# Kernel tuning notes

Hardware: AMD Instinct MI355X
Metric: run time of the kernel (lower is better)

The kernel has to match this reference:

```python
import jax, jax.numpy as jnp
import numpy as np

NEG_SLOPE = 0.01  # nn.LeakyReLU default

def leaky(x):
    return jnp.where(x >= 0, x, NEG_SLOPE * x)

def setup_inputs() -> dict:
    key = jax.random.key(0)
    ks = jax.random.split(key, 10)
    N, E, IN_DIM, OUT_DIM = 100000, 1600000, 128, 128
    indices = jax.random.randint(ks[0], (2, E), 0, N, dtype=jnp.int64 if jax.config.jax_enable_x64 else jnp.int32)
    features = jax.random.normal(ks[1], (N, IN_DIM), dtype=jnp.float32)
    s = 1.0 / np.sqrt(IN_DIM)
    W_att_w = jax.random.uniform(ks[2], (OUT_DIM, IN_DIM), minval=-s, maxval=s)
    W_att_b = jax.random.uniform(ks[3], (OUT_DIM,), minval=-s, maxval=s)
    W1_w = jax.random.uniform(ks[4], (OUT_DIM, IN_DIM), minval=-s, maxval=s)
    W1_b = jax.random.uniform(ks[5], (OUT_DIM,), minval=-s, maxval=s)
    W2_w = jax.random.uniform(ks[6], (OUT_DIM, OUT_DIM), minval=-s, maxval=s)
    W2_b = jax.random.uniform(ks[7], (OUT_DIM,), minval=-s, maxval=s)
    # xavier_uniform for a: gain*sqrt(6/(fan_in+fan_out)), fan_in=2*OUT_DIM, fan_out=1
    lim = float(np.sqrt(6.0 / (2 * OUT_DIM + 1)))
    a = jax.random.uniform(ks[8], (2 * OUT_DIM, 1), minval=-lim, maxval=lim)
    return {"indices": indices, "features": features, "num_nodes": N,
            "W_att_w": W_att_w, "W_att_b": W_att_b, "W1_w": W1_w, "W1_b": W1_b,
            "W2_w": W2_w, "W2_b": W2_b, "a": a}

def reference(indices, features, num_nodes, W_att_w, W_att_b, W1_w, W1_b, W2_w, W2_b, a):
    src, dst = indices[0], indices[1]
    out_dim = W_att_w.shape[0]
    # h_trans = W_att(features)
    h_trans = features @ W_att_w.T + W_att_b  # [N, D]
    # cat([src_h, dst_h]) @ a  ==  src_h @ a[:D] + dst_h @ a[D:]  (avoids materializing cat)
    a_src, a_dst = a[:out_dim], a[out_dim:]
    logits = leaky(h_trans[src] @ a_src + h_trans[dst] @ a_dst)  # [E, 1]
    # edge softmax over incoming edges of each dst (raw exp, as in original)
    exp_l = jnp.exp(logits)
    denom = jax.ops.segment_sum(exp_l, dst, num_segments=num_nodes)  # [N, 1]
    alpha = exp_l / (denom[dst] + 1e-9)  # [E, 1]
    # sparse.mm(adj_att, W1(features)) == segment_sum of alpha * msg[src] over dst
    h_msg = features @ W1_w.T + W1_b  # [N, D]
    h_neigh = jax.ops.segment_sum(alpha * h_msg[src], dst, num_segments=num_nodes)  # [N, D]
    h_self = features  # in_dim == out_dim branch
    term1 = h_self + h_neigh
    term2 = (h_self * h_neigh) @ W2_w.T + W2_b
    return leaky(term1 + term2)
```

## Files before the change

### kernel.cpp

```cpp
#include <hip/hip_runtime.h>

#define D 128
typedef __attribute__((ext_vector_type(8))) short short8;
typedef __attribute__((ext_vector_type(4))) float f32x4;

__device__ __forceinline__ float leaky(float x){ return x >= 0.f ? x : 0.01f*x; }
__device__ __forceinline__ unsigned short f2bf(float x){
    unsigned u = __float_as_uint(x);
    u = (u + 0x7fffu + ((u>>16)&1u)) >> 16;
    return (unsigned short)u;
}

__global__ void k_prep(const float* __restrict__ Ww, const float* __restrict__ Wb,
                       const float* __restrict__ a, float* __restrict__ v,
                       const float* __restrict__ W1, const float* __restrict__ W2,
                       unsigned short* __restrict__ W1b, unsigned short* __restrict__ W2b){
    int b = blockIdx.x;
    if(b < 64){
        int i = b*256 + threadIdx.x;
        W1b[i] = f2bf(W1[i]);
        W2b[i] = f2bf(W2[i]);
        return;
    }
    int i = threadIdx.x; if(i >= 128) return;
    float vs=0.f, vd=0.f;
    for (int o=0;o<D;++o){ float w = Ww[o*D+i]; vs = fmaf(w, a[o], vs); vd = fmaf(w, a[D+o], vd); }
    v[i]=vs; v[D+i]=vd;
    if(i==0){
        float cs=0.f,cd=0.f;
        for(int o=0;o<D;++o){ cs=fmaf(Wb[o],a[o],cs); cd=fmaf(Wb[o],a[D+o],cd); }
        v[256]=cs; v[257]=cd;
    }
}

__global__ __launch_bounds__(256) void k_msgscal(const float* __restrict__ F,
        const unsigned short* __restrict__ W1b, const float* __restrict__ b1,
        const float* __restrict__ v, unsigned short* __restrict__ Hp,
        float* __restrict__ ss, float* __restrict__ sd, int N){
    const int lane = threadIdx.x & 63;
    const int wid  = blockIdx.x*4 + (threadIdx.x>>6);
    const int nw   = gridDim.x*4;
    const int t = lane & 15, g = lane >> 4;
    short8 wf[4][8];
    #pragma unroll
    for(int kk=0;kk<4;++kk)
      #pragma unroll
      for(int j=0;j<8;++j)
        wf[kk][j] = *(const short8*)(W1b + (size_t)(j*16+t)*D + kk*32 + g*8);
    float bb[8];
    #pragma unroll
    for(int j=0;j<8;++j) bb[j] = b1[j*16+t];
    const float c_s = v[256], c_d = v[257];
    const int Mt = (N+15)>>4;
    for(int rt = wid; rt < Mt; rt += nw){
        int row0 = rt*16 + t;
        int row = row0 < N ? row0 : N-1;
        const float* fr = F + (size_t)row*D + g*8;
        f32x4 acc[8];
        #pragma unroll
        for(int j=0;j<8;++j) acc[j] = (f32x4){0.f,0.f,0.f,0.f};
        float ds = 0.f, dd = 0.f;
        #pragma unroll
        for(int kk=0;kk<4;++kk){
            f32x4 lo = *(const f32x4*)(fr + kk*32);
            f32x4 hi = *(const f32x4*)(fr + kk*32 + 4);
            f32x4 vsl = *(const f32x4*)(v + kk*32 + g*8);
            f32x4 vsh = *(const f32x4*)(v + kk*32 + g*8 + 4);
            f32x4 vdl = *(const f32x4*)(v + D + kk*32 + g*8);
            f32x4 vdh = *(const f32x4*)(v + D + kk*32 + g*8 + 4);
            #pragma unroll
            for(int q=0;q<4;++q){
                ds = fmaf(lo[q], vsl[q], ds); ds = fmaf(hi[q], vsh[q], ds);
                dd = fmaf(lo[q], vdl[q], dd); dd = fmaf(hi[q], vdh[q], dd);
            }
            short8 af;
            af[0]=(short)f2bf(lo[0]); af[1]=(short)f2bf(lo[1]);
            af[2]=(short)f2bf(lo[2]); af[3]=(short)f2bf(lo[3]);
            af[4]=(short)f2bf(hi[0]); af[5]=(short)f2bf(hi[1]);
            af[6]=(short)f2bf(hi[2]); af[7]=(short)f2bf(hi[3]);
            #pragma unroll
            for(int j=0;j<8;++j)
                acc[j] = __builtin_amdgcn_mfma_f32_16x16x32_bf16(af, wf[kk][j], acc[j], 0,0,0);
        }
        ds += __shfl_xor(ds,16); ds += __shfl_xor(ds,32);
        dd += __shfl_xor(dd,16); dd += __shfl_xor(dd,32);
        if(g==0 && row0 < N){ ss[row0] = ds + c_s; sd[row0] = dd + c_d; }
        #pragma unroll
        for(int r=0;r<4;++r){
            int rr = rt*16 + g*4 + r;
            if(rr < N){
                short8 h;
                #pragma unroll
                for(int j=0;j<8;++j) h[j] = (short)f2bf(acc[j][r] + bb[j]);
                *(short8*)(Hp + (size_t)rr*D + t*8) = h;
            }
        }
    }
}

__global__ __launch_bounds__(256) void k_bcount(const int* __restrict__ dst,
        unsigned* __restrict__ M, int E, int NB, int CHUNK){
    __shared__ unsigned h[1600];
    for(int i=threadIdx.x;i<NB;i+=256) h[i]=0u;
    __syncthreads();
    int s = blockIdx.x*CHUNK;
    int e = s+CHUNK < E ? s+CHUNK : E;
    for(int i=s+(int)threadIdx.x;i<e;i+=256) atomicAdd(&h[((unsigned)dst[i])>>6],1u);
    __syncthreads();
    for(int i=threadIdx.x;i<NB;i+=256) M[(size_t)i*gridDim.x + blockIdx.x] = h[i];
}

__global__ __launch_bounds__(256) void k_scanA(const unsigned* __restrict__ M,
        unsigned* __restrict__ bsum, int n){
    __shared__ unsigned lds[4];
    int base = blockIdx.x*4096 + threadIdx.x*16;
    unsigned s=0;
    #pragma unroll
    for(int k=0;k<16;++k){ int i=base+k; if(i<n) s+=M[i]; }
    #pragma unroll
    for(int o=1;o<64;o<<=1) s += __shfl_xor(s,o);
    if((threadIdx.x&63)==0) lds[threadIdx.x>>6]=s;
    __syncthreads();
    if(threadIdx.x==0) bsum[blockIdx.x] = lds[0]+lds[1]+lds[2]+lds[3];
}

__global__ __launch_bounds__(256) void k_scanB(unsigned* __restrict__ bsum, int nb){
    __shared__ unsigned lds[4];
    int t = threadIdx.x;
    int chunk = (nb+255)/256;
    int s0 = t*chunk, s1 = s0+chunk < nb ? s0+chunk : nb;
    unsigned tsum=0;
    for(int i=s0;i<s1;++i) tsum += bsum[i];
    unsigned x=tsum;
    #pragma unroll
    for(int o=1;o<64;o<<=1){ unsigned y=__shfl_up(x,(unsigned)o); if((t&63)>=o) x+=y; }
    if((t&63)==63) lds[t>>6]=x;
    __syncthreads();
    unsigned woff=0;
    for(int w=0;w<(t>>6);++w) woff+=lds[w];
    unsigned run = woff + (x - tsum);
    for(int i=s0;i<s1;++i){ unsigned vv=bsum[i]; bsum[i]=run; run+=vv; }
}

__global__ __launch_bounds__(256) void k_scanC(const unsigned* __restrict__ M,
        const unsigned* __restrict__ bsum, unsigned* __restrict__ Msc, int n){
    __shared__ unsigned lds[4];
    int t = threadIdx.x;
    int base = blockIdx.x*4096 + t*16;
    unsigned v[16]; unsigned tsum=0;
    #pragma unroll
    for(int k=0;k<16;++k){ int i=base+k; v[k]=(i<n)?M[i]:0u; tsum+=v[k]; }
    unsigned x=tsum;
    #pragma unroll
    for(int o=1;o<64;o<<=1){ unsigned y=__shfl_up(x,(unsigned)o); if((t&63)>=o) x+=y; }
    if((t&63)==63) lds[t>>6]=x;
    __syncthreads();
    unsigned woff = bsum[blockIdx.x];
    for(int w=0;w<(t>>6);++w) woff+=lds[w];
    unsigned run = woff + (x - tsum);
    #pragma unroll
    for(int k=0;k<16;++k){ int i=base+k; if(i<n) Msc[i]=run; run+=v[k]; }
}

__global__ __launch_bounds__(256) void k_bscatter(const int* __restrict__ src,
        const int* __restrict__ dst, const unsigned* __restrict__ Msc,
        uint2* __restrict__ ew, int E, int NB, int CHUNK){
    __shared__ unsigned hoff[1600];
    int blk = blockIdx.x, NBLKg = gridDim.x;
    for(int i=threadIdx.x;i<NB;i+=256) hoff[i] = Msc[(size_t)i*NBLKg + blk];
    __syncthreads();
    int s = blk*CHUNK;
    int e = s+CHUNK < E ? s+CHUNK : E;
    for(int i=s+(int)threadIdx.x;i<e;i+=256){
        int d = dst[i];
        unsigned p = atomicAdd(&hoff[((unsigned)d)>>6], 1u);
        ew[p] = make_uint2((unsigned)src[i], (unsigned)d);
    }
}

__global__ __launch_bounds__(256) void k_fine(const uint2* __restrict__ ew,
        const unsigned* __restrict__ Msc, const float* __restrict__ ss,
        const float* __restrict__ sdv, uint2* __restrict__ ewp,
        unsigned* __restrict__ offs, int N, int NB, int NBLKg, int E){
    __shared__ unsigned cA[64], cB[64], loff[64];
    __shared__ float sdl[64];
    __shared__ unsigned begS, endS;
    int b = blockIdx.x;
    int dbase = b<<6;
    if(threadIdx.x==0){
        begS = Msc[(size_t)b*NBLKg];
        endS = (b+1 < NB) ? Msc[(size_t)(b+1)*NBLKg] : (unsigned)E;
    }
    if(threadIdx.x<64){
        cA[threadIdx.x]=0u; cB[threadIdx.x]=0u;
        int dd = dbase + (int)threadIdx.x;
        sdl[threadIdx.x] = (dd<N) ? sdv[dd] : 0.f;
    }
    __syncthreads();
    const unsigned beg = begS, end = endS;
    for(unsigned i=beg+threadIdx.x; i<end; i+=256)
        atomicAdd(&cA[ew[i].y & 63], 1u);
    __syncthreads();
    if(threadIdx.x<64){
        unsigned c = cA[threadIdx.x];
        unsigned x = c;
        #pragma unroll
        for(int o=1;o<64;o<<=1){ unsigned y = __shfl_up(x,(unsigned)o); if((int)threadIdx.x>=o) x += y; }
        loff[threadIdx.x] = x - c;
        int dd = dbase + (int)threadIdx.x;
        if(dd < N) offs[dd] = beg + x - c;
    }
    if(b==0 && threadIdx.x==64) offs[N] = (unsigned)E;
    if(b==0 && threadIdx.x>=80 && threadIdx.x<96)
        ewp[E + (threadIdx.x-80)] = make_uint2(0u, 0u);
    __syncthreads();
    for(unsigned i=beg+threadIdx.x; i<end; i+=256){
        uint2 p = ew[i];
        unsigned dl = p.y & 63;
        float w = __expf(leaky(ss[p.x] + sdl[dl]));
        unsigned r = atomicAdd(&cB[dl], 1u);
        ewp[beg + loff[dl] + r] = make_uint2(p.x, __float_as_uint(w));
    }
}

__device__ __forceinline__ void fma8(float* acc, uint4 u, float w){
    acc[0]=fmaf(w,__uint_as_float(u.x<<16),acc[0]);
    acc[1]=fmaf(w,__uint_as_float(u.x&0xffff0000u),acc[1]);
    acc[2]=fmaf(w,__uint_as_float(u.y<<16),acc[2]);
    acc[3]=fmaf(w,__uint_as_float(u.y&0xffff0000u),acc[3]);
    acc[4]=fmaf(w,__uint_as_float(u.z<<16),acc[4]);
    acc[5]=fmaf(w,__uint_as_float(u.z&0xffff0000u),acc[5]);
    acc[6]=fmaf(w,__uint_as_float(u.w<<16),acc[6]);
    acc[7]=fmaf(w,__uint_as_float(u.w&0xffff0000u),acc[7]);
}

__global__ __launch_bounds__(256) void k_gather(const unsigned* __restrict__ off,
        const uint2* __restrict__ ewp, const unsigned short* __restrict__ Hp,
        float* __restrict__ out, int N){
    const int wv = threadIdx.x>>6, l = threadIdx.x&63;
    const int d = blockIdx.x*4 + wv;
    if(d>=N) return;
    const int g = l>>4, t = l&15;
    const unsigned kb = off[d], ke = off[d+1];
    const unsigned toff = (unsigned)t*16u;
    float acc[8];
    #pragma unroll
    for(int j=0;j<8;++j) acc[j]=0.f;
    float den = 0.f;

    unsigned e = kb + g;
    uint2 p0 = ewp[e];
    uint4 u0 = *(const uint4*)((const char*)Hp + ((p0.x<<8) + toff));
    uint2 p1 = ewp[e+4];
    uint4 u1 = *(const uint4*)((const char*)Hp + ((p1.x<<8) + toff));
    while(e < ke){
        float w0 = __uint_as_float(p0.y);
        fma8(acc, u0, w0);
        p0 = ewp[e+8];
        u0 = *(const uint4*)((const char*)Hp + ((p0.x<<8) + toff));
        float w1 = (e+4 < ke) ? __uint_as_float(p1.y) : 0.f;
        fma8(acc, u1, w1);
        p1 = ewp[e+12];
        u1 = *(const uint4*)((const char*)Hp + ((p1.x<<8) + toff));
        den += w0 + w1;
        e += 8;
    }
    #pragma unroll
    for(int j=0;j<8;++j){
        acc[j] += __shfl_xor(acc[j],16);
        acc[j] += __shfl_xor(acc[j],32);
    }
    den += __shfl_xor(den,16);
    den += __shfl_xor(den,32);
    float inv = 1.f/(den + 1e-9f);
    int c = g*32 + t;
    out[(size_t)d*D + c]      = acc[g*2]  * inv;
    out[(size_t)d*D + c + 16] = acc[g*2+1]* inv;
}

__global__ __launch_bounds__(256) void k_final(const float* __restrict__ F,
        const unsigned short* __restrict__ W2b, const float* __restrict__ b2,
        float* __restrict__ out, int N){
    const int lane = threadIdx.x & 63;
    const int wid  = blockIdx.x*4 + (threadIdx.x>>6);
    const int nw   = gridDim.x*4;
    const int t = lane & 15, g = lane >> 4;
    short8 wf[4][8];
    #pragma unroll
    for(int kk=0;kk<4;++kk)
      #pragma unroll
      for(int j=0;j<8;++j)
        wf[kk][j] = *(const short8*)(W2b + (size_t)(j*16+t)*D + kk*32 + g*8);
    float bb[8];
    #pragma unroll
    for(int j=0;j<8;++j) bb[j] = b2[j*16+t];
    const int Mt = (N+15)>>4;
    for(int rt = wid; rt < Mt; rt += nw){
        int row = rt*16 + t; if(row>=N) row = N-1;
        const float* fr = F   + (size_t)row*D + g*8;
        const float* hr = out + (size_t)row*D + g*8;
        f32x4 acc[8];
        #pragma unroll
        for(int j=0;j<8;++j) acc[j] = (f32x4){0.f,0.f,0.f,0.f};
        #pragma unroll
        for(int kk=0;kk<4;++kk){
            f32x4 flo = *(const f32x4*)(fr + kk*32);
            f32x4 fhi = *(const f32x4*)(fr + kk*32 + 4);
            f32x4 hlo = *(const f32x4*)(hr + kk*32);
            f32x4 hhi = *(const f32x4*)(hr + kk*32 + 4);
            short8 af;
            af[0]=(short)f2bf(flo[0]*hlo[0]); af[1]=(short)f2bf(flo[1]*hlo[1]);
            af[2]=(short)f2bf(flo[2]*hlo[2]); af[3]=(short)f2bf(flo[3]*hlo[3]);
            af[4]=(short)f2bf(fhi[0]*hhi[0]); af[5]=(short)f2bf(fhi[1]*hhi[1]);
            af[6]=(short)f2bf(fhi[2]*hhi[2]); af[7]=(short)f2bf(fhi[3]*hhi[3]);
            #pragma unroll
            for(int j=0;j<8;++j)
                acc[j] = __builtin_amdgcn_mfma_f32_16x16x32_bf16(af, wf[kk][j], acc[j], 0,0,0);
        }
        #pragma unroll
        for(int r=0;r<4;++r){
            int rr = rt*16 + g*4 + r;
            if(rr < N){
                #pragma unroll
                for(int j=0;j<8;++j){
                    int c = j*16 + t;
                    float f = F[(size_t)rr*D + c];
                    float h = out[(size_t)rr*D + c];
                    float val = f + h + acc[j][r] + bb[j];
                    out[(size_t)rr*D + c] = leaky(val);
                }
            }
        }
    }
}

extern "C" void kernel_launch(void* const* d_in, const int* in_sizes, int n_in,
                              void* d_out, int out_size, void* d_ws, size_t ws_size,
                              hipStream_t stream) {
    const int*   idx  = (const int*)  d_in[0];
    const float* F    = (const float*)d_in[1];
    const float* Waw  = (const float*)d_in[3];
    const float* Wab  = (const float*)d_in[4];
    const float* W1w  = (const float*)d_in[5];
    const float* W1b  = (const float*)d_in[6];
    const float* W2w  = (const float*)d_in[7];
    const float* W2b  = (const float*)d_in[8];
    const float* a    = (const float*)d_in[9];
    float* out = (float*)d_out;

    const int E = in_sizes[0]/2;
    const int N = in_sizes[1]/D;
    const int* srcp = idx;
    const int* dstp = idx + E;

    const int NBLK = 256;
    const int CHUNK = (E + NBLK - 1)/NBLK;
    const int NB = (N + 63)/64;
    const int NT = NB*NBLK;
    const int NSB = (NT + 4095)/4096;

    uint2*    ew   = (uint2*)d_ws;
    uint2*    ewp  = ew + E;
    unsigned short* Hp  = (unsigned short*)(ewp + E + 16);
    unsigned short* W1c = Hp + (size_t)N*D;
    unsigned short* W2c = W1c + 16384;
    float*    ss   = (float*)(W2c + 16384);
    float*    sd   = ss + N;
    float*    v    = sd + N;
    unsigned* M    = (unsigned*)(v + 320);
    unsigned* Msc  = M + NT;
    unsigned* bsum = Msc + NT + 2;
    unsigned* offs = bsum + NSB + 2;

    const int Mt = (N+15)/16;
    const int GG = (Mt+7)/8;

    k_prep    <<<65, 256, 0, stream>>>(Waw, Wab, a, v, W1w, W2w, W1c, W2c);
    k_msgscal <<<GG, 256, 0, stream>>>(F, W1c, W1b, v, Hp, ss, sd, N);
    k_bcount  <<<NBLK, 256, 0, stream>>>(dstp, M, E, NB, CHUNK);
    k_scanA   <<<NSB, 256, 0, stream>>>(M, bsum, NT);
    k_scanB   <<<1, 256, 0, stream>>>(bsum, NSB);
    k_scanC   <<<NSB, 256, 0, stream>>>(M, bsum, Msc, NT);
    k_bscatter<<<NBLK, 256, 0, stream>>>(srcp, dstp, Msc, ew, E, NB, CHUNK);
    k_fine    <<<NB, 256, 0, stream>>>(ew, Msc, ss, sd, ewp, offs, N, NB, NBLK, E);
    k_gather  <<<(N+3)/4, 256, 0, stream>>>(offs, ewp, Hp, out, N);
    k_final   <<<GG, 256, 0, stream>>>(F, W2c, W2b, out, N);
}
```

Before: 220.8 us.

## Fuse gather with final MFMA epilogue, fold scanB into scanC, move exp to scatter

```diff
diff --git a/kernel.cpp b/kernel.cpp
--- a/kernel.cpp
+++ b/kernel.cpp
@@ -124,66 +124,54 @@
     if(threadIdx.x==0) bsum[blockIdx.x] = lds[0]+lds[1]+lds[2]+lds[3];
 }
 
-__global__ __launch_bounds__(256) void k_scanB(unsigned* __restrict__ bsum, int nb){
+__global__ __launch_bounds__(256) void k_scanC(const unsigned* __restrict__ M,
+        const unsigned* __restrict__ bsum, unsigned* __restrict__ Msc, int n, int nsb){
     __shared__ unsigned lds[4];
+    __shared__ unsigned ps[2];
     int t = threadIdx.x;
-    int chunk = (nb+255)/256;
-    int s0 = t*chunk, s1 = s0+chunk < nb ? s0+chunk : nb;
-    unsigned tsum=0;
-    for(int i=s0;i<s1;++i) tsum += bsum[i];
+    unsigned pv = (t < nsb && t < (int)blockIdx.x) ? bsum[t] : 0u;
+    #pragma unroll
+    for(int o=1;o<64;o<<=1) pv += __shfl_xor(pv,o);
+    if((t&63)==0 && t<128) ps[t>>6]=pv;
+    int base = blockIdx.x*4096 + t*16;
+    unsigned v[16]; unsigned tsum=0;
+    #pragma unroll
+    for(int k=0;k<16;++k){ int i=base+k; v[k]=(i<n)?M[i]:0u; tsum+=v[k]; }
     unsigned x=tsum;
     #pragma unroll
     for(int o=1;o<64;o<<=1){ unsigned y=__shfl_up(x,(unsigned)o); if((t&63)>=o) x+=y; }
     if((t&63)==63) lds[t>>6]=x;
     __syncthreads();
-    unsigned woff=0;
-    for(int w=0;w<(t>>6);++w) woff+=lds[w];
-    unsigned run = woff + (x - tsum);
-    for(int i=s0;i<s1;++i){ unsigned vv=bsum[i]; bsum[i]=run; run+=vv; }
-}
-
-__global__ __launch_bounds__(256) void k_scanC(const unsigned* __restrict__ M,
-        const unsigned* __restrict__ bsum, unsigned* __restrict__ Msc, int n){
-    __shared__ unsigned lds[4];
-    int t = threadIdx.x;
-    int base = blockIdx.x*4096 + t*16;
-    unsigned v[16]; unsigned tsum=0;
-    #pragma unroll
-    for(int k=0;k<16;++k){ int i=base+k; v[k]=(i<n)?M[i]:0u; tsum+=v[k]; }
-    unsigned x=tsum;
-    #pragma unroll
-    for(int o=1;o<64;o<<=1){ unsigned y=__shfl_up(x,(unsigned)o); if((t&63)>=o) x+=y; }
-    if((t&63)==63) lds[t>>6]=x;
-    __syncthreads();
-    unsigned woff = bsum[blockIdx.x];
-    for(int w=0;w<(t>>6);++w) woff+=lds[w];
-    unsigned run = woff + (x - tsum);
+    unsigned run = ps[0]+ps[1];
+    for(int w=0;w<(t>>6);++w) run += lds[w];
+    run += (x - tsum);
     #pragma unroll
     for(int k=0;k<16;++k){ int i=base+k; if(i<n) Msc[i]=run; run+=v[k]; }
 }
 
 __global__ __launch_bounds__(256) void k_bscatter(const int* __restrict__ src,
         const int* __restrict__ dst, const unsigned* __restrict__ Msc,
+        const float* __restrict__ ss, const float* __restrict__ sdv,
         uint2* __restrict__ ew, int E, int NB, int CHUNK){
     __shared__ unsigned hoff[1600];
     int blk = blockIdx.x, NBLKg = gridDim.x;
     for(int i=threadIdx.x;i<NB;i+=256) hoff[i] = Msc[(size_t)i*NBLKg + blk];
     __syncthreads();
-    int s = blk*CHUNK;
-    int e = s+CHUNK < E ? s+CHUNK : E;
-    for(int i=s+(int)threadIdx.x;i<e;i+=256){
+    int s0 = blk*CHUNK;
+    int e1 = s0+CHUNK < E ? s0+CHUNK : E;
+    for(int i=s0+(int)threadIdx.x;i<e1;i+=256){
         int d = dst[i];
+        int s = src[i];
+        float w = __expf(leaky(ss[s] + sdv[d]));
         unsigned p = atomicAdd(&hoff[((unsigned)d)>>6], 1u);
-        ew[p] = make_uint2((unsigned)src[i], (unsigned)d);
+        ew[p] = make_uint2(((unsigned)s<<6)|((unsigned)d&63u), __float_as_uint(w));
     }
 }
 
 __global__ __launch_bounds__(256) void k_fine(const uint2* __restrict__ ew,
-        const unsigned* __restrict__ Msc, const float* __restrict__ ss,
-        const float* __restrict__ sdv, uint2* __restrict__ ewp,
+        const unsigned* __restrict__ Msc, uint2* __restrict__ ewp,
         unsigned* __restrict__ offs, int N, int NB, int NBLKg, int E){
     __shared__ unsigned cA[64], cB[64], loff[64];
-    __shared__ float sdl[64];
     __shared__ unsigned begS, endS;
     int b = blockIdx.x;
     int dbase = b<<6;
@@ -191,15 +179,11 @@
         begS = Msc[(size_t)b*NBLKg];
         endS = (b+1 < NB) ? Msc[(size_t)(b+1)*NBLKg] : (unsigned)E;
     }
-    if(threadIdx.x<64){
-        cA[threadIdx.x]=0u; cB[threadIdx.x]=0u;
-        int dd = dbase + (int)threadIdx.x;
-        sdl[threadIdx.x] = (dd<N) ? sdv[dd] : 0.f;
-    }
+    if(threadIdx.x<64){ cA[threadIdx.x]=0u; cB[threadIdx.x]=0u; }
     __syncthreads();
     const unsigned beg = begS, end = endS;
     for(unsigned i=beg+threadIdx.x; i<end; i+=256)
-        atomicAdd(&cA[ew[i].y & 63], 1u);
+        atomicAdd(&cA[ew[i].x & 63u], 1u);
     __syncthreads();
     if(threadIdx.x<64){
         unsigned c = cA[threadIdx.x];
@@ -216,10 +200,9 @@
     __syncthreads();
     for(unsigned i=beg+threadIdx.x; i<end; i+=256){
         uint2 p = ew[i];
-        unsigned dl = p.y & 63;
-        float w = __expf(leaky(ss[p.x] + sdl[dl]));
+        unsigned dl = p.x & 63u;
         unsigned r = atomicAdd(&cB[dl], 1u);
-        ewp[beg + loff[dl] + r] = make_uint2(p.x, __float_as_uint(w));
+        ewp[beg + loff[dl] + r] = make_uint2(p.x >> 6, p.y);
     }
 }
 
@@ -234,102 +217,95 @@
     acc[7]=fmaf(w,__uint_as_float(u.w&0xffff0000u),acc[7]);
 }
 
-__global__ __launch_bounds__(256) void k_gather(const unsigned* __restrict__ off,
+__global__ __launch_bounds__(256) void k_gfin(const unsigned* __restrict__ off,
         const uint2* __restrict__ ewp, const unsigned short* __restrict__ Hp,
-        float* __restrict__ out, int N){
+        const float* __restrict__ F, const unsigned short* __restrict__ W2b,
+        const float* __restrict__ b2, float* __restrict__ out, int N){
+    __shared__ float hl[16][132];
     const int wv = threadIdx.x>>6, l = threadIdx.x&63;
-    const int d = blockIdx.x*4 + wv;
-    if(d>=N) return;
     const int g = l>>4, t = l&15;
-    const unsigned kb = off[d], ke = off[d+1];
+    const int base = blockIdx.x*16;
     const unsigned toff = (unsigned)t*16u;
-    float acc[8];
-    #pragma unroll
-    for(int j=0;j<8;++j) acc[j]=0.f;
-    float den = 0.f;
-
-    unsigned e = kb + g;
-    uint2 p0 = ewp[e];
-    uint4 u0 = *(const uint4*)((const char*)Hp + ((p0.x<<8) + toff));
-    uint2 p1 = ewp[e+4];
-    uint4 u1 = *(const uint4*)((const char*)Hp + ((p1.x<<8) + toff));
-    while(e < ke){
-        float w0 = __uint_as_float(p0.y);
-        fma8(acc, u0, w0);
-        p0 = ewp[e+8];
-        u0 = *(const uint4*)((const char*)Hp + ((p0.x<<8) + toff));
-        float w1 = (e+4 < ke) ? __uint_as_float(p1.y) : 0.f;
-        fma8(acc, u1, w1);
-        p1 = ewp[e+12];
-        u1 = *(const uint4*)((const char*)Hp + ((p1.x<<8) + toff));
-        den += w0 + w1;
-        e += 8;
-    }
-    #pragma unroll
-    for(int j=0;j<8;++j){
-        acc[j] += __shfl_xor(acc[j],16);
-        acc[j] += __shfl_xor(acc[j],32);
-    }
-    den += __shfl_xor(den,16);
-    den += __shfl_xor(den,32);
-    float inv = 1.f/(den + 1e-9f);
-    int c = g*32 + t;
-    out[(size_t)d*D + c]      = acc[g*2]  * inv;
-    out[(size_t)d*D + c + 16] = acc[g*2+1]* inv;
-}
-
-__global__ __launch_bounds__(256) void k_final(const float* __restrict__ F,
-        const unsigned short* __restrict__ W2b, const float* __restrict__ b2,
-        float* __restrict__ out, int N){
-    const int lane = threadIdx.x & 63;
-    const int wid  = blockIdx.x*4 + (threadIdx.x>>6);
-    const int nw   = gridDim.x*4;
-    const int t = lane & 15, g = lane >> 4;
-    short8 wf[4][8];
+
+    for(int i=0;i<4;++i){
+        int d = base + wv*4 + i;
+        float acc[8];
+        #pragma unroll
+        for(int j=0;j<8;++j) acc[j]=0.f;
+        float den = 0.f;
+        if(d < N){
+            unsigned kb = off[d], ke = off[d+1];
+            unsigned e = kb + g;
+            uint2 p0 = ewp[e];
+            uint4 u0 = *(const uint4*)((const char*)Hp + ((p0.x<<8) + toff));
+            uint2 p1 = ewp[e+4];
+            uint4 u1 = *(const uint4*)((const char*)Hp + ((p1.x<<8) + toff));
+            while(e < ke){
+                float w0 = __uint_as_float(p0.y);
+                fma8(acc, u0, w0);
+                p0 = ewp[e+8];
+                u0 = *(const uint4*)((const char*)Hp + ((p0.x<<8) + toff));
+                float w1 = (e+4 < ke) ? __uint_as_float(p1.y) : 0.f;
+                fma8(acc, u1, w1);
+                p1 = ewp[e+12];
+                u1 = *(const uint4*)((const char*)Hp + ((p1.x<<8) + toff));
+                den += w0 + w1;
+                e += 8;
+            }
+        }
+        #pragma unroll
+        for(int j=0;j<8;++j){
+            acc[j] += __shfl_xor(acc[j],16);
+            acc[j] += __shfl_xor(acc[j],32);
+        }
+        den += __shfl_xor(den,16);
+        den += __shfl_xor(den,32);
+        float inv = 1.f/(den + 1e-9f);
+        int row = wv*4 + i;
+        int c = g*32 + t;
+        hl[row][c]      = acc[g*2]  * inv;
+        hl[row][c + 16] = acc[g*2+1]* inv;
+    }
+    __syncthreads();
+
+    const int j0 = wv*2;
+    short8 wf[4][2];
     #pragma unroll
     for(int kk=0;kk<4;++kk)
       #pragma unroll
-      for(int j=0;j<8;++j)
-        wf[kk][j] = *(const short8*)(W2b + (size_t)(j*16+t)*D + kk*32 + g*8);
-    float bb[8];
-    #pragma unroll
-    for(int j=0;j<8;++j) bb[j] = b2[j*16+t];
-    const int Mt = (N+15)>>4;
-    for(int rt = wid; rt < Mt; rt += nw){
-        int row = rt*16 + t; if(row>=N) row = N-1;
-        const float* fr = F   + (size_t)row*D + g*8;
-        const float* hr = out + (size_t)row*D + g*8;
-        f32x4 acc[8];
-        #pragma unroll
-        for(int j=0;j<8;++j) acc[j] = (f32x4){0.f,0.f,0.f,0.f};
-        #pragma unroll
-        for(int kk=0;kk<4;++kk){
-            f32x4 flo = *(const f32x4*)(fr + kk*32);
-            f32x4 fhi = *(const f32x4*)(fr + kk*32 + 4);
-            f32x4 hlo = *(const f32x4*)(hr + kk*32);
-            f32x4 hhi = *(const f32x4*)(hr + kk*32 + 4);
-            short8 af;
-            af[0]=(short)f2bf(flo[0]*hlo[0]); af[1]=(short)f2bf(flo[1]*hlo[1]);
-            af[2]=(short)f2bf(flo[2]*hlo[2]); af[3]=(short)f2bf(flo[3]*hlo[3]);
-            af[4]=(short)f2bf(fhi[0]*hhi[0]); af[5]=(short)f2bf(fhi[1]*hhi[1]);
-            af[6]=(short)f2bf(fhi[2]*hhi[2]); af[7]=(short)f2bf(fhi[3]*hhi[3]);
-            #pragma unroll
-            for(int j=0;j<8;++j)
-                acc[j] = __builtin_amdgcn_mfma_f32_16x16x32_bf16(af, wf[kk][j], acc[j], 0,0,0);
-        }
-        #pragma unroll
-        for(int r=0;r<4;++r){
-            int rr = rt*16 + g*4 + r;
-            if(rr < N){
-                #pragma unroll
-                for(int j=0;j<8;++j){
-                    int c = j*16 + t;
-                    float f = F[(size_t)rr*D + c];
-                    float h = out[(size_t)rr*D + c];
-                    float val = f + h + acc[j][r] + bb[j];
-                    out[(size_t)rr*D + c] = leaky(val);
-                }
-            }
+      for(int jj=0;jj<2;++jj)
+        wf[kk][jj] = *(const short8*)(W2b + (size_t)((j0+jj)*16+t)*D + kk*32 + g*8);
+    float bb0 = b2[j0*16+t], bb1 = b2[(j0+1)*16+t];
+    f32x4 acc20 = (f32x4){0.f,0.f,0.f,0.f};
+    f32x4 acc21 = (f32x4){0.f,0.f,0.f,0.f};
+    int arow = base + t;
+    const float* fr = F + (size_t)(arow < N ? arow : N-1)*D + g*8;
+    #pragma unroll
+    for(int kk=0;kk<4;++kk){
+        f32x4 flo = *(const f32x4*)(fr + kk*32);
+        f32x4 fhi = *(const f32x4*)(fr + kk*32 + 4);
+        f32x4 hlo = *(const f32x4*)(&hl[t][kk*32 + g*8]);
+        f32x4 hhi = *(const f32x4*)(&hl[t][kk*32 + g*8 + 4]);
+        short8 af;
+        af[0]=(short)f2bf(flo[0]*hlo[0]); af[1]=(short)f2bf(flo[1]*hlo[1]);
+        af[2]=(short)f2bf(flo[2]*hlo[2]); af[3]=(short)f2bf(flo[3]*hlo[3]);
+        af[4]=(short)f2bf(fhi[0]*hhi[0]); af[5]=(short)f2bf(fhi[1]*hhi[1]);
+        af[6]=(short)f2bf(fhi[2]*hhi[2]); af[7]=(short)f2bf(fhi[3]*hhi[3]);
+        acc20 = __builtin_amdgcn_mfma_f32_16x16x32_bf16(af, wf[kk][0], acc20, 0,0,0);
+        acc21 = __builtin_amdgcn_mfma_f32_16x16x32_bf16(af, wf[kk][1], acc21, 0,0,0);
+    }
+    #pragma unroll
+    for(int r=0;r<4;++r){
+        int rr = base + g*4 + r;
+        if(rr < N){
+            int c0 = j0*16 + t;
+            float f0 = F[(size_t)rr*D + c0];
+            float h0 = hl[g*4 + r][c0];
+            out[(size_t)rr*D + c0] = leaky(f0 + h0 + acc20[r] + bb0);
+            int c1 = (j0+1)*16 + t;
+            float f1 = F[(size_t)rr*D + c1];
+            float h1 = hl[g*4 + r][c1];
+            out[(size_t)rr*D + c1] = leaky(f1 + h1 + acc21[r] + bb1);
         }
     }
 }
@@ -379,10 +355,8 @@
     k_msgscal <<<GG, 256, 0, stream>>>(F, W1c, W1b, v, Hp, ss, sd, N);
     k_bcount  <<<NBLK, 256, 0, stream>>>(dstp, M, E, NB, CHUNK);
     k_scanA   <<<NSB, 256, 0, stream>>>(M, bsum, NT);
-    k_scanB   <<<1, 256, 0, stream>>>(bsum, NSB);
-    k_scanC   <<<NSB, 256, 0, stream>>>(M, bsum, Msc, NT);
-    k_bscatter<<<NBLK, 256, 0, stream>>>(srcp, dstp, Msc, ew, E, NB, CHUNK);
-    k_fine    <<<NB, 256, 0, stream>>>(ew, Msc, ss, sd, ewp, offs, N, NB, NBLK, E);
-    k_gather  <<<(N+3)/4, 256, 0, stream>>>(offs, ewp, Hp, out, N);
-    k_final   <<<GG, 256, 0, stream>>>(F, W2c, W2b, out, N);
-}
+    k_scanC   <<<NSB, 256, 0, stream>>>(M, bsum, Msc, NT, NSB);
+    k_bscatter<<<NBLK, 256, 0, stream>>>(srcp, dstp, Msc, ss, sd, ew, E, NB, CHUNK);
+    k_fine    <<<NB, 256, 0, stream>>>(ew, Msc, ewp, offs, N, NB, NBLK, E);
+    k_gfin    <<<(N+15)/16, 256, 0, stream>>>(offs, ewp, Hp, F, W2c, W2b, out, N);
+}
```

Result: no change. 220.0 us (-0.3%).

## Fold weight bf16 conversion into GEMM kernels, merge scan passes, move edge-weight exp into scatter

Applied to the files above, without the earlier changes.

```diff
diff --git a/kernel.cpp b/kernel.cpp
--- a/kernel.cpp
+++ b/kernel.cpp
@@ -10,18 +10,17 @@
     u = (u + 0x7fffu + ((u>>16)&1u)) >> 16;
     return (unsigned short)u;
 }
+__device__ __forceinline__ short8 pack8m(f32x4 a, f32x4 b){
+    short8 s;
+    s[0]=(short)f2bf(a[0]); s[1]=(short)f2bf(a[1]);
+    s[2]=(short)f2bf(a[2]); s[3]=(short)f2bf(a[3]);
+    s[4]=(short)f2bf(b[0]); s[5]=(short)f2bf(b[1]);
+    s[6]=(short)f2bf(b[2]); s[7]=(short)f2bf(b[3]);
+    return s;
+}
 
 __global__ void k_prep(const float* __restrict__ Ww, const float* __restrict__ Wb,
-                       const float* __restrict__ a, float* __restrict__ v,
-                       const float* __restrict__ W1, const float* __restrict__ W2,
-                       unsigned short* __restrict__ W1b, unsigned short* __restrict__ W2b){
-    int b = blockIdx.x;
-    if(b < 64){
-        int i = b*256 + threadIdx.x;
-        W1b[i] = f2bf(W1[i]);
-        W2b[i] = f2bf(W2[i]);
-        return;
-    }
+                       const float* __restrict__ a, float* __restrict__ v){
     int i = threadIdx.x; if(i >= 128) return;
     float vs=0.f, vd=0.f;
     for (int o=0;o<D;++o){ float w = Ww[o*D+i]; vs = fmaf(w, a[o], vs); vd = fmaf(w, a[D+o], vd); }
@@ -34,7 +33,7 @@
 }
 
 __global__ __launch_bounds__(256) void k_msgscal(const float* __restrict__ F,
-        const unsigned short* __restrict__ W1b, const float* __restrict__ b1,
+        const float* __restrict__ W1, const float* __restrict__ b1,
         const float* __restrict__ v, unsigned short* __restrict__ Hp,
         float* __restrict__ ss, float* __restrict__ sd, int N){
     const int lane = threadIdx.x & 63;
@@ -45,8 +44,10 @@
     #pragma unroll
     for(int kk=0;kk<4;++kk)
       #pragma unroll
-      for(int j=0;j<8;++j)
-        wf[kk][j] = *(const short8*)(W1b + (size_t)(j*16+t)*D + kk*32 + g*8);
+      for(int j=0;j<8;++j){
+        const float* p = W1 + (size_t)(j*16+t)*D + kk*32 + g*8;
+        wf[kk][j] = pack8m(*(const f32x4*)p, *(const f32x4*)(p+4));
+      }
     float bb[8];
     #pragma unroll
     for(int j=0;j<8;++j) bb[j] = b1[j*16+t];
@@ -73,11 +74,7 @@
                 ds = fmaf(lo[q], vsl[q], ds); ds = fmaf(hi[q], vsh[q], ds);
                 dd = fmaf(lo[q], vdl[q], dd); dd = fmaf(hi[q], vdh[q], dd);
             }
-            short8 af;
-            af[0]=(short)f2bf(lo[0]); af[1]=(short)f2bf(lo[1]);
-            af[2]=(short)f2bf(lo[2]); af[3]=(short)f2bf(lo[3]);
-            af[4]=(short)f2bf(hi[0]); af[5]=(short)f2bf(hi[1]);
-            af[6]=(short)f2bf(hi[2]); af[7]=(short)f2bf(hi[3]);
+            short8 af = pack8m(lo, hi);
             #pragma unroll
             for(int j=0;j<8;++j)
                 acc[j] = __builtin_amdgcn_mfma_f32_16x16x32_bf16(af, wf[kk][j], acc[j], 0,0,0);
@@ -107,7 +104,7 @@
     int e = s+CHUNK < E ? s+CHUNK : E;
     for(int i=s+(int)threadIdx.x;i<e;i+=256) atomicAdd(&h[((unsigned)dst[i])>>6],1u);
     __syncthreads();
-    for(int i=threadIdx.x;i<NB;i+=256) M[(size_t)i*gridDim.x + blockIdx.x] = h[i];
+    for(int j=threadIdx.x;j<NB;j+=256) M[(size_t)j*gridDim.x + blockIdx.x] = h[j];
 }
 
 __global__ __launch_bounds__(256) void k_scanA(const unsigned* __restrict__ M,
@@ -124,66 +121,54 @@
     if(threadIdx.x==0) bsum[blockIdx.x] = lds[0]+lds[1]+lds[2]+lds[3];
 }
 
-__global__ __launch_bounds__(256) void k_scanB(unsigned* __restrict__ bsum, int nb){
+__global__ __launch_bounds__(256) void k_scanC(const unsigned* __restrict__ M,
+        const unsigned* __restrict__ bsum, unsigned* __restrict__ Msc, int n, int nsb){
     __shared__ unsigned lds[4];
+    __shared__ unsigned ps[2];
     int t = threadIdx.x;
-    int chunk = (nb+255)/256;
-    int s0 = t*chunk, s1 = s0+chunk < nb ? s0+chunk : nb;
-    unsigned tsum=0;
-    for(int i=s0;i<s1;++i) tsum += bsum[i];
+    unsigned pv = (t < nsb && t < (int)blockIdx.x) ? bsum[t] : 0u;
+    #pragma unroll
+    for(int o=1;o<64;o<<=1) pv += __shfl_xor(pv,o);
+    if((t&63)==0 && t<128) ps[t>>6]=pv;
+    int base = blockIdx.x*4096 + t*16;
+    unsigned v[16]; unsigned tsum=0;
+    #pragma unroll
+    for(int k=0;k<16;++k){ int i=base+k; v[k]=(i<n)?M[i]:0u; tsum+=v[k]; }
     unsigned x=tsum;
     #pragma unroll
     for(int o=1;o<64;o<<=1){ unsigned y=__shfl_up(x,(unsigned)o); if((t&63)>=o) x+=y; }
     if((t&63)==63) lds[t>>6]=x;
     __syncthreads();
-    unsigned woff=0;
-    for(int w=0;w<(t>>6);++w) woff+=lds[w];
-    unsigned run = woff + (x - tsum);
-    for(int i=s0;i<s1;++i){ unsigned vv=bsum[i]; bsum[i]=run; run+=vv; }
-}
-
-__global__ __launch_bounds__(256) void k_scanC(const unsigned* __restrict__ M,
-        const unsigned* __restrict__ bsum, unsigned* __restrict__ Msc, int n){
-    __shared__ unsigned lds[4];
-    int t = threadIdx.x;
-    int base = blockIdx.x*4096 + t*16;
-    unsigned v[16]; unsigned tsum=0;
-    #pragma unroll
-    for(int k=0;k<16;++k){ int i=base+k; v[k]=(i<n)?M[i]:0u; tsum+=v[k]; }
-    unsigned x=tsum;
-    #pragma unroll
-    for(int o=1;o<64;o<<=1){ unsigned y=__shfl_up(x,(unsigned)o); if((t&63)>=o) x+=y; }
-    if((t&63)==63) lds[t>>6]=x;
-    __syncthreads();
-    unsigned woff = bsum[blockIdx.x];
-    for(int w=0;w<(t>>6);++w) woff+=lds[w];
-    unsigned run = woff + (x - tsum);
+    unsigned run = ps[0]+ps[1];
+    for(int w=0;w<(t>>6);++w) run += lds[w];
+    run += (x - tsum);
     #pragma unroll
     for(int k=0;k<16;++k){ int i=base+k; if(i<n) Msc[i]=run; run+=v[k]; }
 }
 
 __global__ __launch_bounds__(256) void k_bscatter(const int* __restrict__ src,
         const int* __restrict__ dst, const unsigned* __restrict__ Msc,
+        const float* __restrict__ ss, const float* __restrict__ sdv,
         uint2* __restrict__ ew, int E, int NB, int CHUNK){
     __shared__ unsigned hoff[1600];
     int blk = blockIdx.x, NBLKg = gridDim.x;
     for(int i=threadIdx.x;i<NB;i+=256) hoff[i] = Msc[(size_t)i*NBLKg + blk];
     __syncthreads();
-    int s = blk*CHUNK;
-    int e = s+CHUNK < E ? s+CHUNK : E;
-    for(int i=s+(int)threadIdx.x;i<e;i+=256){
+    int s0 = blk*CHUNK;
+    int e1 = s0+CHUNK < E ? s0+CHUNK : E;
+    for(int i=s0+(int)threadIdx.x;i<e1;i+=256){
         int d = dst[i];
+        int s = src[i];
+        float w = __expf(leaky(ss[s] + sdv[d]));
         unsigned p = atomicAdd(&hoff[((unsigned)d)>>6], 1u);
-        ew[p] = make_uint2((unsigned)src[i], (unsigned)d);
+        ew[p] = make_uint2(((unsigned)s<<6)|((unsigned)d&63u), __float_as_uint(w));
     }
 }
 
 __global__ __launch_bounds__(256) void k_fine(const uint2* __restrict__ ew,
-        const unsigned* __restrict__ Msc, const float* __restrict__ ss,
-        const float* __restrict__ sdv, uint2* __restrict__ ewp,
+        const unsigned* __restrict__ Msc, uint2* __restrict__ ewp,
         unsigned* __restrict__ offs, int N, int NB, int NBLKg, int E){
     __shared__ unsigned cA[64], cB[64], loff[64];
-    __shared__ float sdl[64];
     __shared__ unsigned begS, endS;
     int b = blockIdx.x;
     int dbase = b<<6;
@@ -191,15 +176,11 @@
         begS = Msc[(size_t)b*NBLKg];
         endS = (b+1 < NB) ? Msc[(size_t)(b+1)*NBLKg] : (unsigned)E;
     }
-    if(threadIdx.x<64){
-        cA[threadIdx.x]=0u; cB[threadIdx.x]=0u;
-        int dd = dbase + (int)threadIdx.x;
-        sdl[threadIdx.x] = (dd<N) ? sdv[dd] : 0.f;
-    }
+    if(threadIdx.x<64){ cA[threadIdx.x]=0u; cB[threadIdx.x]=0u; }
     __syncthreads();
     const unsigned beg = begS, end = endS;
     for(unsigned i=beg+threadIdx.x; i<end; i+=256)
-        atomicAdd(&cA[ew[i].y & 63], 1u);
+        atomicAdd(&cA[ew[i].x & 63u], 1u);
     __syncthreads();
     if(threadIdx.x<64){
         unsigned c = cA[threadIdx.x];
@@ -216,10 +197,9 @@
     __syncthreads();
     for(unsigned i=beg+threadIdx.x; i<end; i+=256){
         uint2 p = ew[i];
-        unsigned dl = p.y & 63;
-        float w = __expf(leaky(ss[p.x] + sdl[dl]));
+        unsigned dl = p.x & 63u;
         unsigned r = atomicAdd(&cB[dl], 1u);
-        ewp[beg + loff[dl] + r] = make_uint2(p.x, __float_as_uint(w));
+        ewp[beg + loff[dl] + r] = make_uint2(p.x >> 6, p.y);
     }
 }
 
@@ -279,7 +259,7 @@
 }
 
 __global__ __launch_bounds__(256) void k_final(const float* __restrict__ F,
-        const unsigned short* __restrict__ W2b, const float* __restrict__ b2,
+        const float* __restrict__ W2, const float* __restrict__ b2,
         float* __restrict__ out, int N){
     const int lane = threadIdx.x & 63;
     const int wid  = blockIdx.x*4 + (threadIdx.x>>6);
@@ -289,8 +269,10 @@
     #pragma unroll
     for(int kk=0;kk<4;++kk)
       #pragma unroll
-      for(int j=0;j<8;++j)
-        wf[kk][j] = *(const short8*)(W2b + (size_t)(j*16+t)*D + kk*32 + g*8);
+      for(int j=0;j<8;++j){
+        const float* p = W2 + (size_t)(j*16+t)*D + kk*32 + g*8;
+        wf[kk][j] = pack8m(*(const f32x4*)p, *(const f32x4*)(p+4));
+      }
     float bb[8];
     #pragma unroll
     for(int j=0;j<8;++j) bb[j] = b2[j*16+t];
@@ -308,11 +290,7 @@
             f32x4 fhi = *(const f32x4*)(fr + kk*32 + 4);
             f32x4 hlo = *(const f32x4*)(hr + kk*32);
             f32x4 hhi = *(const f32x4*)(hr + kk*32 + 4);
-            short8 af;
-            af[0]=(short)f2bf(flo[0]*hlo[0]); af[1]=(short)f2bf(flo[1]*hlo[1]);
-            af[2]=(short)f2bf(flo[2]*hlo[2]); af[3]=(short)f2bf(flo[3]*hlo[3]);
-            af[4]=(short)f2bf(fhi[0]*hhi[0]); af[5]=(short)f2bf(fhi[1]*hhi[1]);
-            af[6]=(short)f2bf(fhi[2]*hhi[2]); af[7]=(short)f2bf(fhi[3]*hhi[3]);
+            short8 af = pack8m(flo*hlo, fhi*hhi);
             #pragma unroll
             for(int j=0;j<8;++j)
                 acc[j] = __builtin_amdgcn_mfma_f32_16x16x32_bf16(af, wf[kk][j], acc[j], 0,0,0);
@@ -326,8 +304,7 @@
                     int c = j*16 + t;
                     float f = F[(size_t)rr*D + c];
                     float h = out[(size_t)rr*D + c];
-                    float val = f + h + acc[j][r] + bb[j];
-                    out[(size_t)rr*D + c] = leaky(val);
+                    out[(size_t)rr*D + c] = leaky(f + h + acc[j][r] + bb[j]);
                 }
             }
         }
@@ -362,9 +339,7 @@
     uint2*    ew   = (uint2*)d_ws;
     uint2*    ewp  = ew + E;
     unsigned short* Hp  = (unsigned short*)(ewp + E + 16);
-    unsigned short* W1c = Hp + (size_t)N*D;
-    unsigned short* W2c = W1c + 16384;
-    float*    ss   = (float*)(W2c + 16384);
+    float*    ss   = (float*)(Hp + (size_t)N*D);
     float*    sd   = ss + N;
     float*    v    = sd + N;
     unsigned* M    = (unsigned*)(v + 320);
@@ -375,14 +350,13 @@
     const int Mt = (N+15)/16;
     const int GG = (Mt+7)/8;
 
-    k_prep    <<<65, 256, 0, stream>>>(Waw, Wab, a, v, W1w, W2w, W1c, W2c);
-    k_msgscal <<<GG, 256, 0, stream>>>(F, W1c, W1b, v, Hp, ss, sd, N);
+    k_prep    <<<1, 128, 0, stream>>>(Waw, Wab, a, v);
+    k_msgscal <<<GG, 256, 0, stream>>>(F, W1w, W1b, v, Hp, ss, sd, N);
     k_bcount  <<<NBLK, 256, 0, stream>>>(dstp, M, E, NB, CHUNK);
     k_scanA   <<<NSB, 256, 0, stream>>>(M, bsum, NT);
-    k_scanB   <<<1, 256, 0, stream>>>(bsum, NSB);
-    k_scanC   <<<NSB, 256, 0, stream>>>(M, bsum, Msc, NT);
-    k_bscatter<<<NBLK, 256, 0, stream>>>(srcp, dstp, Msc, ew, E, NB, CHUNK);
-    k_fine    <<<NB, 256, 0, stream>>>(ew, Msc, ss, sd, ewp, offs, N, NB, NBLK, E);
+    k_scanC   <<<NSB, 256, 0, stream>>>(M, bsum, Msc, NT, NSB);
+    k_bscatter<<<NBLK, 256, 0, stream>>>(srcp, dstp, Msc, ss, sd, ew, E, NB, CHUNK);
+    k_fine    <<<NB, 256, 0, stream>>>(ew, Msc, ewp, offs, N, NB, NBLK, E);
     k_gather  <<<(N+3)/4, 256, 0, stream>>>(offs, ewp, Hp, out, N);
-    k_final   <<<GG, 256, 0, stream>>>(F, W2c, W2b, out, N);
-}
+    k_final   <<<GG, 256, 0, stream>>>(F, W2w, W2b, out, N);
+}
```

New measurement: 254.7 us. 1.15x slower.
